# Kernel optimization log

Measured on AMD Instinct MI355X. Metric: run time of the kernel, lower is better.

Reference implementation:

```python
import jax, jax.numpy as jnp
import numpy as np

N_NODES = 50000
N_EDGES = 800000
D_IN = 128
D_HID = 128


def _sage_conv(x, src, dst, W_l, b_l, W_r, num_nodes):
    # PyG SAGEConv (mean aggr): out = lin_l(mean_{j in N(i)} x_j) + lin_r(x_i)
    msgs = x[src]  # [E, d] irregular gather
    agg = jax.ops.segment_sum(msgs, dst, num_segments=num_nodes)  # [N, d]
    cnt = jax.ops.segment_sum(jnp.ones((dst.shape[0], 1), x.dtype), dst, num_segments=num_nodes)
    agg = agg / jnp.maximum(cnt, 1.0)  # mean over in-neighbors
    return agg @ W_l.T + b_l + x @ W_r.T


def setup_inputs() -> dict:
    key = jax.random.key(0)
    ks = jax.random.split(key, 8)
    x = jax.random.normal(ks[0], (N_NODES, D_IN), dtype=jnp.float32)
    edge_index = jax.random.randint(ks[1], (2, N_EDGES), 0, N_NODES, dtype=jnp.int64)
    s0 = 1.0 / np.sqrt(D_IN)
    s1 = 1.0 / np.sqrt(D_HID)
    return {
        "x": x,
        "edge_index": edge_index,
        "W_l0": jax.random.uniform(ks[2], (D_HID, D_IN), jnp.float32, -s0, s0),
        "b_l0": jnp.zeros((D_HID,), jnp.float32),
        "W_r0": jax.random.uniform(ks[3], (D_HID, D_IN), jnp.float32, -s0, s0),
        "W_l1": jax.random.uniform(ks[4], (D_HID, D_HID), jnp.float32, -s1, s1),
        "b_l1": jnp.zeros((D_HID,), jnp.float32),
        "W_r1": jax.random.uniform(ks[5], (D_HID, D_HID), jnp.float32, -s1, s1),
    }


def reference(x, edge_index, W_l0, b_l0, W_r0, W_l1, b_l1, W_r1):
    src, dst = edge_index[0], edge_index[1]
    n = x.shape[0]
    # layer 0 + ReLU (dropout is identity at inference)
    h = _sage_conv(x, src, dst, W_l0, b_l0, W_r0, n)
    h = jax.nn.relu(h)
    # layer 1 (no activation on last layer)
    out = _sage_conv(h, src, dst, W_l1, b_l1, W_r1, n)
    return out
```

## Files before the change

kernel.cpp:

```cpp
#include <hip/hip_runtime.h>


typedef __attribute__((ext_vector_type(8))) short short8;
typedef __attribute__((ext_vector_type(4))) float f32x4;

#define DEV __device__ __forceinline__

DEV unsigned short f2b(float f) {
  unsigned u = __builtin_bit_cast(unsigned, f);
  u += 0x7fffu + ((u >> 16) & 1u);
  return (unsigned short)(u >> 16);
}
DEV float b2f(unsigned short h) {
  unsigned u = ((unsigned)h) << 16;
  return __builtin_bit_cast(float, u);
}

constexpr int N_NODES = 50000;
constexpr int N_EDGES = 800000;
constexpr int D = 128;
constexpr int NBUCK = (N_NODES + 255) / 256;
constexpr int BCAP = 5120;
constexpr int NBIN = 784;
constexpr int EPB = (N_EDGES + NBIN - 1) / NBIN;
constexpr int NCONV = (N_NODES * D / 4) / 256;
constexpr int NPREP = (2 * 32 * 128) / 256;

__global__ __launch_bounds__(256) void setup_kernel(
    const float* __restrict__ x, unsigned short* __restrict__ xb,
    const float* __restrict__ Wl0, const float* __restrict__ Wr0,
    const float* __restrict__ Wl1, const float* __restrict__ Wr1,
    unsigned short* __restrict__ Bf,
    const int* __restrict__ src, const int* __restrict__ dst,
    int* __restrict__ g_bcnt, unsigned* __restrict__ staging) {
  __shared__ int cnt[NBUCK];
  __shared__ int cur[NBUCK];
  int bid = blockIdx.x;
  int t = threadIdx.x;

  if (bid < NBIN) {
    for (int i = t; i < NBUCK; i += 256) cnt[i] = 0;
    __syncthreads();
    int beg = bid * EPB;
    int end = min(beg + EPB, N_EDGES);
    for (int e = beg + t; e < end; e += 256) {
      atomicAdd(&cnt[dst[e] >> 8], 1);
    }
    __syncthreads();
    for (int i = t; i < NBUCK; i += 256) {
      cur[i] = atomicAdd(&g_bcnt[i], cnt[i]);
    }
    __syncthreads();
    for (int e = beg + t; e < end; e += 256) {
      int d = dst[e];
      int b = d >> 8;
      int p = atomicAdd(&cur[b], 1);
      if (p >= BCAP) p = BCAP - 1;
      staging[b * BCAP + p] = ((unsigned)(d & 255) << 16) | (unsigned)src[e];
    }
    return;
  }
  if (bid < NBIN + NCONV) {
    int i = (bid - NBIN) * 256 + t;
    f32x4 v = ((const f32x4*)x)[i];
    uint2 o;
    o.x = (unsigned)f2b(v.x) | ((unsigned)f2b(v.y) << 16);
    o.y = (unsigned)f2b(v.z) | ((unsigned)f2b(v.w) << 16);
    ((uint2*)xb)[i] = o;
    return;
  }
  int f = (bid - NBIN - NCONV) * 256 + t;
  int layer = f >> 12;
  int kchunk = (f >> 7) & 31;
  int n = f & 127;
  const float* W;
  if (layer == 0) W = (kchunk < 16) ? Wl0 : Wr0;
  else            W = (kchunk < 16) ? Wl1 : Wr1;
  int k = (kchunk & 15) * 8;
  const f32x4* row = (const f32x4*)(W + n * D + k);
  f32x4 a = row[0], b = row[1];
  uint4 pk;
  pk.x = (unsigned)f2b(a.x) | ((unsigned)f2b(a.y) << 16);
  pk.y = (unsigned)f2b(a.z) | ((unsigned)f2b(a.w) << 16);
  pk.z = (unsigned)f2b(b.x) | ((unsigned)f2b(b.y) << 16);
  pk.w = (unsigned)f2b(b.z) | ((unsigned)f2b(b.w) << 16);
  *(uint4*)(Bf + (size_t)f * 8) = pk;
}

__global__ __launch_bounds__(1024) void fill2_kernel(const unsigned* __restrict__ staging,
                                                     const int* __restrict__ g_bcnt,
                                                     int* __restrict__ offs,
                                                     int* __restrict__ csr) {
  __shared__ int cnts[256];
  __shared__ int tmp[256];
  __shared__ int hist[256];
  __shared__ int cur[256];
  __shared__ int sh_n, sh_bb;
  int b = blockIdx.x;
  int t = threadIdx.x;
  if (t < 256) {
    int c = (t < NBUCK) ? g_bcnt[t] : 0;
    cnts[t] = c;
    tmp[t] = c;
    hist[t] = 0;
  }
  __syncthreads();
  if (t < 256) {
    for (int off = 1; off < 256; off <<= 1) {
      int u = (t >= off) ? tmp[t - off] : 0;
      __syncthreads();
      tmp[t] += u;
      __syncthreads();
    }
  } else {
    for (int off = 1; off < 256; off <<= 1) { __syncthreads(); __syncthreads(); }
  }
  if (t == 0) {
    sh_n = cnts[b];
    sh_bb = tmp[b] - cnts[b];
  }
  __syncthreads();
  int n = sh_n;
  int bb = sh_bb;
  if (b == 0 && t == 0) offs[N_NODES] = N_EDGES;

  const unsigned* st = staging + b * BCAP;
  for (int e = t; e < n; e += 1024) atomicAdd(&hist[st[e] >> 16], 1);
  __syncthreads();
  if (t < 256) {
    int v = hist[t];
    tmp[t] = v;
    __syncthreads();
    for (int off = 1; off < 256; off <<= 1) {
      int u = (t >= off) ? tmp[t - off] : 0;
      __syncthreads();
      tmp[t] += u;
      __syncthreads();
    }
    int excl = tmp[t] - v;
    int node = b * 256 + t;
    if (node < N_NODES) offs[node] = bb + excl;
    cur[t] = bb + excl;
  } else {
    __syncthreads();
    for (int off = 1; off < 256; off <<= 1) { __syncthreads(); __syncthreads(); }
  }
  __syncthreads();
  for (int e = t; e < n; e += 1024) {
    unsigned pk = st[e];
    int p = atomicAdd(&cur[pk >> 16], 1);
    csr[p] = (int)(pk & 0xffffu);
  }
}

__global__ void agg_kernel(const unsigned short* __restrict__ feat,
                           const int* __restrict__ csr_src,
                           const int* __restrict__ offs,
                           unsigned short* __restrict__ out) {
  int w = (int)((blockIdx.x * blockDim.x + threadIdx.x) >> 6);
  int lane = threadIdx.x & 63;
  if (w >= N_NODES) return;
  int s = offs[w], e = offs[w + 1];
  const unsigned* f = (const unsigned*)feat;
  float ax = 0.f, ay = 0.f;
  int k = s;
  for (; k + 4 <= e; k += 4) {
    int s0 = csr_src[k], s1 = csr_src[k + 1], s2 = csr_src[k + 2], s3 = csr_src[k + 3];
    unsigned u0 = f[s0 * 64 + lane];
    unsigned u1 = f[s1 * 64 + lane];
    unsigned u2 = f[s2 * 64 + lane];
    unsigned u3 = f[s3 * 64 + lane];
    ax += b2f((unsigned short)u0) + b2f((unsigned short)u1) +
          b2f((unsigned short)u2) + b2f((unsigned short)u3);
    ay += b2f((unsigned short)(u0 >> 16)) + b2f((unsigned short)(u1 >> 16)) +
          b2f((unsigned short)(u2 >> 16)) + b2f((unsigned short)(u3 >> 16));
  }
  for (; k < e; ++k) {
    unsigned u = f[csr_src[k] * 64 + lane];
    ax += b2f((unsigned short)u);
    ay += b2f((unsigned short)(u >> 16));
  }
  float inv = 1.0f / (float)max(e - s, 1);
  unsigned o = (unsigned)f2b(ax * inv) | ((unsigned)f2b(ay * inv) << 16);
  ((unsigned*)out)[w * 64 + lane] = o;
}

__global__ __launch_bounds__(256) void gemm_kernel(
    const unsigned short* __restrict__ Aagg,
    const unsigned short* __restrict__ Afeat,
    const unsigned short* __restrict__ Bf,
    const float* __restrict__ bias,
    float* __restrict__ out_f32,
    unsigned short* __restrict__ out_bf16,
    int relu_bf16) {
  int wave = threadIdx.x >> 6;
  int lane = threadIdx.x & 63;
  int ml = lane & 15;
  int quad = lane >> 4;
  int node0 = blockIdx.x * 128 + wave * 32;

  int ar0 = node0 + ml;       if (ar0 >= N_NODES) ar0 = N_NODES - 1;
  int ar1 = node0 + 16 + ml;  if (ar1 >= N_NODES) ar1 = N_NODES - 1;

  f32x4 acc[2][8];
#pragma unroll
  for (int m = 0; m < 2; ++m)
#pragma unroll
    for (int t = 0; t < 8; ++t) acc[m][t] = (f32x4){0.f, 0.f, 0.f, 0.f};

  const short8* bf8 = (const short8*)Bf;
#pragma unroll
  for (int mat = 0; mat < 2; ++mat) {
    const unsigned short* A = mat ? Afeat : Aagg;
    const short8* a0 = (const short8*)(A + (size_t)ar0 * D);
    const short8* a1 = (const short8*)(A + (size_t)ar1 * D);
    int kbase = mat * 16;
#pragma unroll
    for (int kc = 0; kc < 4; ++kc) {
      short8 af0 = a0[kc * 4 + quad];
      short8 af1 = a1[kc * 4 + quad];
      const short8* brow = bf8 + (kbase + kc * 4 + quad) * 128;
#pragma unroll
      for (int nt = 0; nt < 8; ++nt) {
        short8 bfr = brow[nt * 16 + ml];
        acc[0][nt] = __builtin_amdgcn_mfma_f32_16x16x32_bf16(af0, bfr, acc[0][nt], 0, 0, 0);
        acc[1][nt] = __builtin_amdgcn_mfma_f32_16x16x32_bf16(af1, bfr, acc[1][nt], 0, 0, 0);
      }
    }
  }

#pragma unroll
  for (int tile = 0; tile < 2; ++tile) {
#pragma unroll
    for (int nt = 0; nt < 8; ++nt) {
      int col = nt * 16 + ml;
      float bv = bias[col];
#pragma unroll
      for (int r = 0; r < 4; ++r) {
        int node = node0 + tile * 16 + quad * 4 + r;
        if (node >= N_NODES) continue;
        float v = acc[tile][nt][r] + bv;
        if (relu_bf16) {
          v = v > 0.f ? v : 0.f;
          out_bf16[(size_t)node * D + col] = f2b(v);
        } else {
          out_f32[(size_t)node * D + col] = v;
        }
      }
    }
  }
}

extern "C" void kernel_launch(void* const* d_in, const int* in_sizes, int n_in,
                              void* d_out, int out_size, void* d_ws, size_t ws_size,
                              hipStream_t stream) {
  const float* x   = (const float*)d_in[0];
  const int*   ei  = (const int*)d_in[1];
  const float* Wl0 = (const float*)d_in[2];
  const float* bl0 = (const float*)d_in[3];
  const float* Wr0 = (const float*)d_in[4];
  const float* Wl1 = (const float*)d_in[5];
  const float* bl1 = (const float*)d_in[6];
  const float* Wr1 = (const float*)d_in[7];
  float* out = (float*)d_out;

  char* ws = (char*)d_ws;
  size_t o = 0;
  auto carve = [&](size_t bytes) {
    char* p = ws + o;
    o += bytes;
    o = (o + 255) & ~(size_t)255;
    return p;
  };
  int* offs       = (int*)carve((size_t)(N_NODES + 1) * 4);
  int* csr        = (int*)carve((size_t)N_EDGES * 4);
  int* g_bcnt     = (int*)carve((size_t)NBUCK * 4);
  unsigned* staging = (unsigned*)carve((size_t)NBUCK * BCAP * 4);
  unsigned short* Bf   = (unsigned short*)carve((size_t)2 * 32 * 128 * 8 * 2);
  unsigned short* xb   = (unsigned short*)carve((size_t)N_NODES * D * 2);
  unsigned short* aggb = (unsigned short*)carve((size_t)N_NODES * D * 2);
  unsigned short* hb   = (unsigned short*)carve((size_t)N_NODES * D * 2);

  const int* srcp = ei;
  const int* dstp = ei + N_EDGES;

  hipMemsetAsync(g_bcnt, 0, (size_t)NBUCK * 4, stream);
  setup_kernel<<<NBIN + NCONV + NPREP, 256, 0, stream>>>(
      x, xb, Wl0, Wr0, Wl1, Wr1, Bf, srcp, dstp, g_bcnt, staging);
  fill2_kernel<<<NBUCK, 1024, 0, stream>>>(staging, g_bcnt, offs, csr);

  const int GEMM_BLOCKS = (N_NODES + 127) / 128;
  agg_kernel<<<(N_NODES + 3) / 4, 256, 0, stream>>>(xb, csr, offs, aggb);
  gemm_kernel<<<GEMM_BLOCKS, 256, 0, stream>>>(aggb, xb, Bf, bl0, nullptr, hb, 1);
  agg_kernel<<<(N_NODES + 3) / 4, 256, 0, stream>>>(hb, csr, offs, aggb);
  gemm_kernel<<<GEMM_BLOCKS, 256, 0, stream>>>(aggb, hb, Bf + 32 * 128 * 8, bl1,
                                               out, nullptr, 0);
}
```

Before: 240.9 us.

## Fuse neighbor mean aggregation and GEMM into one per-layer kernel

Merges the separate aggregation and GEMM kernels into a single kernel per layer. Each block aggregates 64 nodes into padded shared memory, then runs MFMA on that tile, with the four waves split across M and N halves. This removes the global round-trip of the aggregated bf16 buffer and two kernel launches. In exchange each wave handles 16 nodes sequentially in the gather phase, and the grid has fewer, longer blocks, which can reduce latency hiding.

```diff
diff --git a/kernel.cpp b/kernel.cpp
--- a/kernel.cpp
+++ b/kernel.cpp
@@ -25,6 +25,7 @@
 constexpr int EPB = (N_EDGES + NBIN - 1) / NBIN;
 constexpr int NCONV = (N_NODES * D / 4) / 256;
 constexpr int NPREP = (2 * 32 * 128) / 256;
+constexpr int ROWQ = 136;
 
 __global__ __launch_bounds__(256) void setup_kernel(
     const float* __restrict__ x, unsigned short* __restrict__ xb,
@@ -153,75 +154,82 @@
   }
 }
 
-__global__ void agg_kernel(const unsigned short* __restrict__ feat,
-                           const int* __restrict__ csr_src,
-                           const int* __restrict__ offs,
-                           unsigned short* __restrict__ out) {
-  int w = (int)((blockIdx.x * blockDim.x + threadIdx.x) >> 6);
-  int lane = threadIdx.x & 63;
-  if (w >= N_NODES) return;
-  int s = offs[w], e = offs[w + 1];
-  const unsigned* f = (const unsigned*)feat;
-  float ax = 0.f, ay = 0.f;
-  int k = s;
-  for (; k + 4 <= e; k += 4) {
-    int s0 = csr_src[k], s1 = csr_src[k + 1], s2 = csr_src[k + 2], s3 = csr_src[k + 3];
-    unsigned u0 = f[s0 * 64 + lane];
-    unsigned u1 = f[s1 * 64 + lane];
-    unsigned u2 = f[s2 * 64 + lane];
-    unsigned u3 = f[s3 * 64 + lane];
-    ax += b2f((unsigned short)u0) + b2f((unsigned short)u1) +
-          b2f((unsigned short)u2) + b2f((unsigned short)u3);
-    ay += b2f((unsigned short)(u0 >> 16)) + b2f((unsigned short)(u1 >> 16)) +
-          b2f((unsigned short)(u2 >> 16)) + b2f((unsigned short)(u3 >> 16));
-  }
-  for (; k < e; ++k) {
-    unsigned u = f[csr_src[k] * 64 + lane];
-    ax += b2f((unsigned short)u);
-    ay += b2f((unsigned short)(u >> 16));
-  }
-  float inv = 1.0f / (float)max(e - s, 1);
-  unsigned o = (unsigned)f2b(ax * inv) | ((unsigned)f2b(ay * inv) << 16);
-  ((unsigned*)out)[w * 64 + lane] = o;
-}
-
-__global__ __launch_bounds__(256) void gemm_kernel(
-    const unsigned short* __restrict__ Aagg,
-    const unsigned short* __restrict__ Afeat,
+__global__ __launch_bounds__(256, 4) void fused_layer_kernel(
+    const unsigned short* __restrict__ feat,
+    const int* __restrict__ csr_src,
+    const int* __restrict__ offs,
     const unsigned short* __restrict__ Bf,
     const float* __restrict__ bias,
     float* __restrict__ out_f32,
     unsigned short* __restrict__ out_bf16,
     int relu_bf16) {
-  int wave = threadIdx.x >> 6;
+  __shared__ unsigned short Asm[64 * ROWQ];
+
+  int v = threadIdx.x >> 6;
   int lane = threadIdx.x & 63;
+  int node0 = blockIdx.x * 64;
+
+  const unsigned* f32rows = (const unsigned*)feat;
+  for (int j = 0; j < 16; ++j) {
+    int ln = v * 16 + j;
+    int node = node0 + ln;
+    if (node >= N_NODES) break;
+    int s = offs[node], e = offs[node + 1];
+    float ax = 0.f, ay = 0.f;
+    int k = s;
+    for (; k + 4 <= e; k += 4) {
+      int s0 = csr_src[k], s1 = csr_src[k + 1], s2 = csr_src[k + 2], s3 = csr_src[k + 3];
+      unsigned u0 = f32rows[s0 * 64 + lane];
+      unsigned u1 = f32rows[s1 * 64 + lane];
+      unsigned u2 = f32rows[s2 * 64 + lane];
+      unsigned u3 = f32rows[s3 * 64 + lane];
+      ax += b2f((unsigned short)u0) + b2f((unsigned short)u1) +
+            b2f((unsigned short)u2) + b2f((unsigned short)u3);
+      ay += b2f((unsigned short)(u0 >> 16)) + b2f((unsigned short)(u1 >> 16)) +
+            b2f((unsigned short)(u2 >> 16)) + b2f((unsigned short)(u3 >> 16));
+    }
+    for (; k < e; ++k) {
+      unsigned u = f32rows[csr_src[k] * 64 + lane];
+      ax += b2f((unsigned short)u);
+      ay += b2f((unsigned short)(u >> 16));
+    }
+    float inv = 1.0f / (float)max(e - s, 1);
+    ((unsigned*)Asm)[ln * (ROWQ / 2) + lane] =
+        (unsigned)f2b(ax * inv) | ((unsigned)f2b(ay * inv) << 16);
+  }
+  __syncthreads();
+
   int ml = lane & 15;
   int quad = lane >> 4;
-  int node0 = blockIdx.x * 128 + wave * 32;
-
-  int ar0 = node0 + ml;       if (ar0 >= N_NODES) ar0 = N_NODES - 1;
-  int ar1 = node0 + 16 + ml;  if (ar1 >= N_NODES) ar1 = N_NODES - 1;
-
-  f32x4 acc[2][8];
+  int mt = v & 1;
+  int nh = v >> 1;
+
+  int r0 = mt * 32 + ml;
+  int r1 = mt * 32 + 16 + ml;
+  int g0 = node0 + r0; if (g0 >= N_NODES) g0 = N_NODES - 1;
+  int g1 = node0 + r1; if (g1 >= N_NODES) g1 = N_NODES - 1;
+
+  const short8* lA0 = (const short8*)(Asm + r0 * ROWQ);
+  const short8* lA1 = (const short8*)(Asm + r1 * ROWQ);
+  const short8* gA0 = (const short8*)(feat + (size_t)g0 * D);
+  const short8* gA1 = (const short8*)(feat + (size_t)g1 * D);
+  const short8* bf8 = (const short8*)Bf;
+
+  f32x4 acc[2][4];
 #pragma unroll
   for (int m = 0; m < 2; ++m)
 #pragma unroll
-    for (int t = 0; t < 8; ++t) acc[m][t] = (f32x4){0.f, 0.f, 0.f, 0.f};
-
-  const short8* bf8 = (const short8*)Bf;
+    for (int t = 0; t < 4; ++t) acc[m][t] = (f32x4){0.f, 0.f, 0.f, 0.f};
+
 #pragma unroll
   for (int mat = 0; mat < 2; ++mat) {
-    const unsigned short* A = mat ? Afeat : Aagg;
-    const short8* a0 = (const short8*)(A + (size_t)ar0 * D);
-    const short8* a1 = (const short8*)(A + (size_t)ar1 * D);
-    int kbase = mat * 16;
 #pragma unroll
     for (int kc = 0; kc < 4; ++kc) {
-      short8 af0 = a0[kc * 4 + quad];
-      short8 af1 = a1[kc * 4 + quad];
-      const short8* brow = bf8 + (kbase + kc * 4 + quad) * 128;
-#pragma unroll
-      for (int nt = 0; nt < 8; ++nt) {
+      short8 af0 = mat ? gA0[kc * 4 + quad] : lA0[kc * 4 + quad];
+      short8 af1 = mat ? gA1[kc * 4 + quad] : lA1[kc * 4 + quad];
+      const short8* brow = bf8 + (mat * 16 + kc * 4 + quad) * 128 + nh * 64;
+#pragma unroll
+      for (int nt = 0; nt < 4; ++nt) {
         short8 bfr = brow[nt * 16 + ml];
         acc[0][nt] = __builtin_amdgcn_mfma_f32_16x16x32_bf16(af0, bfr, acc[0][nt], 0, 0, 0);
         acc[1][nt] = __builtin_amdgcn_mfma_f32_16x16x32_bf16(af1, bfr, acc[1][nt], 0, 0, 0);
@@ -232,19 +240,19 @@
 #pragma unroll
   for (int tile = 0; tile < 2; ++tile) {
 #pragma unroll
-    for (int nt = 0; nt < 8; ++nt) {
-      int col = nt * 16 + ml;
+    for (int nt = 0; nt < 4; ++nt) {
+      int col = nh * 64 + nt * 16 + ml;
       float bv = bias[col];
 #pragma unroll
       for (int r = 0; r < 4; ++r) {
-        int node = node0 + tile * 16 + quad * 4 + r;
+        int node = node0 + mt * 32 + tile * 16 + quad * 4 + r;
         if (node >= N_NODES) continue;
-        float v = acc[tile][nt][r] + bv;
+        float val = acc[tile][nt][r] + bv;
         if (relu_bf16) {
-          v = v > 0.f ? v : 0.f;
-          out_bf16[(size_t)node * D + col] = f2b(v);
+          val = val > 0.f ? val : 0.f;
+          out_bf16[(size_t)node * D + col] = f2b(val);
         } else {
-          out_f32[(size_t)node * D + col] = v;
+          out_f32[(size_t)node * D + col] = val;
         }
       }
     }
@@ -276,10 +284,9 @@
   int* csr        = (int*)carve((size_t)N_EDGES * 4);
   int* g_bcnt     = (int*)carve((size_t)NBUCK * 4);
   unsigned* staging = (unsigned*)carve((size_t)NBUCK * BCAP * 4);
-  unsigned short* Bf   = (unsigned short*)carve((size_t)2 * 32 * 128 * 8 * 2);
-  unsigned short* xb   = (unsigned short*)carve((size_t)N_NODES * D * 2);
-  unsigned short* aggb = (unsigned short*)carve((size_t)N_NODES * D * 2);
-  unsigned short* hb   = (unsigned short*)carve((size_t)N_NODES * D * 2);
+  unsigned short* Bf = (unsigned short*)carve((size_t)2 * 32 * 128 * 8 * 2);
+  unsigned short* xb = (unsigned short*)carve((size_t)N_NODES * D * 2);
+  unsigned short* hb = (unsigned short*)carve((size_t)N_NODES * D * 2);
 
   const int* srcp = ei;
   const int* dstp = ei + N_EDGES;
@@ -289,10 +296,10 @@
       x, xb, Wl0, Wr0, Wl1, Wr1, Bf, srcp, dstp, g_bcnt, staging);
   fill2_kernel<<<NBUCK, 1024, 0, stream>>>(staging, g_bcnt, offs, csr);
 
-  const int GEMM_BLOCKS = (N_NODES + 127) / 128;
-  agg_kernel<<<(N_NODES + 3) / 4, 256, 0, stream>>>(xb, csr, offs, aggb);
-  gemm_kernel<<<GEMM_BLOCKS, 256, 0, stream>>>(aggb, xb, Bf, bl0, nullptr, hb, 1);
-  agg_kernel<<<(N_NODES + 3) / 4, 256, 0, stream>>>(hb, csr, offs, aggb);
-  gemm_kernel<<<GEMM_BLOCKS, 256, 0, stream>>>(aggb, hb, Bf + 32 * 128 * 8, bl1,
-                                               out, nullptr, 0);
-}
+  const int LBLOCKS = (N_NODES + 63) / 64;
+  fused_layer_kernel<<<LBLOCKS, 256, 0, stream>>>(xb, csr, offs, Bf, bl0,
+                                                  nullptr, hb, 1);
+  fused_layer_kernel<<<LBLOCKS, 256, 0, stream>>>(hb, csr, offs,
+                                                  Bf + 32 * 128 * 8, bl1,
+                                                  out, nullptr, 0);
+}
```

Result: slower. 274.5 us (+14.0%).
